# Kernel tuning notes

Measured on AMD Instinct MI355X. Metric: run time of the kernel, lower is better.

Reference implementation:

```python
import jax, jax.numpy as jnp
import numpy as np

ALPHA = 0.01  # LeakyReLU negative slope
NEG_INF = -1e12

def setup_inputs() -> dict:
    key = jax.random.key(0)
    k1, k2, k3, k4 = jax.random.split(key, 4)
    B, N, F_in, F_out = 8, 2048, 256, 128
    inp = jax.random.normal(k1, (B, N, F_in), dtype=jnp.float32)
    adj = jax.random.randint(k2, (B, N, N), 0, 2, dtype=jnp.int32)
    # xavier_uniform with gain=1.414
    limW = 1.414 * np.sqrt(6.0 / (F_in + F_out))
    W = jax.random.uniform(k3, (F_in, F_out), minval=-limW, maxval=limW, dtype=jnp.float32)
    lima = 1.414 * np.sqrt(6.0 / (2 * F_out + 1))
    a = jax.random.uniform(k4, (2 * F_out, 1), minval=-lima, maxval=lima, dtype=jnp.float32)
    return {"inp": inp, "adj": adj, "W": W, "a": a}

def reference(inp, adj, W, a):
    # h: [B, N, F_out]
    h = jnp.matmul(inp, W)
    F_out = W.shape[1]
    # Algebraic split of the attention vector: a = [a1; a2], so
    # e[b,i,j] = leakyrelu(h_i . a1 + h_j . a2)  -- avoids the O(N^2*2F) a_input.
    a1 = a[:F_out, 0]   # [F_out]
    a2 = a[F_out:, 0]   # [F_out]
    s1 = jnp.einsum('bnf,f->bn', h, a1)  # [B, N] source term
    s2 = jnp.einsum('bnf,f->bn', h, a2)  # [B, N] target term
    e = s1[:, :, None] + s2[:, None, :]  # [B, N, N]
    e = jnp.where(e > 0, e, ALPHA * e)   # leaky relu
    scores = jnp.where(adj > 0, e, NEG_INF)
    attention = jax.nn.softmax(scores, axis=2)  # [B, N, N]
    h_prime = jnp.matmul(attention, h)          # [B, N, F_out]
    return jax.nn.relu(h_prime)  # concat=True branch
```

## Files before the change

kernel.cpp:

```cpp
#include <hip/hip_runtime.h>
#include <hip/hip_bf16.h>

#define N_    2048
#define FIN   256
#define FOUT  128
#define ALPHA 0.01f

typedef short bf16x8 __attribute__((ext_vector_type(8)));
typedef float f32x4  __attribute__((ext_vector_type(4)));

static __device__ __forceinline__ unsigned short f2bf(float x) {
    __hip_bfloat16 h = __float2bfloat16(x);
    return *reinterpret_cast<unsigned short*>(&h);
}
static __device__ __forceinline__ float bf2f(unsigned short u) {
    return __uint_as_float(((unsigned)u) << 16);
}

__global__ __launch_bounds__(256) void k_wsplit(
    const float* __restrict__ W, unsigned short* __restrict__ WThi,
    unsigned short* __restrict__ WTlo)
{
    int idx = blockIdx.x * 256 + threadIdx.x;
    int k = idx >> 7, n = idx & 127;
    float w = W[k * 128 + n];
    unsigned short hi = f2bf(w);
    unsigned short lo = f2bf(w - bf2f(hi));
    WThi[n * 256 + k] = hi;
    WTlo[n * 256 + k] = lo;
}

__global__ __launch_bounds__(256) void k_pack(
    const int* __restrict__ adj, unsigned int* __restrict__ mask)
{
    __shared__ unsigned char mb[256];
    int row = blockIdx.x;
    int t = threadIdx.x;
    const int4* a4 = reinterpret_cast<const int4*>(adj + (size_t)row * N_) + 2 * t;
    int4 x = a4[0], y = a4[1];
    unsigned byte =
        (unsigned)(x.x > 0) | ((unsigned)(x.y > 0) << 1) |
        ((unsigned)(x.z > 0) << 2) | ((unsigned)(x.w > 0) << 3) |
        ((unsigned)(y.x > 0) << 4) | ((unsigned)(y.y > 0) << 5) |
        ((unsigned)(y.z > 0) << 6) | ((unsigned)(y.w > 0) << 7);
    int w = t >> 6, cig = t & 63;
    int S = cig >> 2, lg = cig & 3;
    mb[w * 64 + lg * 16 + S] = (unsigned char)byte;
    __syncthreads();
    if (t < 16)
        reinterpret_cast<uint4*>(mask)[row * 16 + t] =
            reinterpret_cast<const uint4*>(mb)[t];
}

__global__ __launch_bounds__(256) void k_lin(
    const float* __restrict__ inp,
    const unsigned short* __restrict__ WThi, const unsigned short* __restrict__ WTlo,
    const float* __restrict__ av, unsigned short* __restrict__ hT,
    float* __restrict__ s1, float* __restrict__ s2)
{
    __shared__ unsigned short Ahi[64 * 256];
    __shared__ unsigned short Alo[64 * 256];

    int g = blockIdx.x;
    int b = g & 7;
    int i0 = (g >> 3) << 6;
    int t = threadIdx.x;

    {
        int row = t >> 2;
        const float* src = inp + ((size_t)(b * N_ + i0 + row)) * FIN + (t & 3) * 64;
#pragma unroll
        for (int gseg = 0; gseg < 8; ++gseg) {
            float4 f0 = *reinterpret_cast<const float4*>(src + gseg * 8);
            float4 f1 = *reinterpret_cast<const float4*>(src + gseg * 8 + 4);
            float f[8] = {f0.x, f0.y, f0.z, f0.w, f1.x, f1.y, f1.z, f1.w};
            bf16x8 hi8, lo8;
#pragma unroll
            for (int e = 0; e < 8; ++e) {
                unsigned short h = f2bf(f[e]);
                hi8[e] = (short)h;
                lo8[e] = (short)f2bf(f[e] - bf2f(h));
            }
            int k = (t & 3) * 64 + gseg * 8;
            int off = (row * 512 + k * 2) ^ ((row & 7) << 4);
            *reinterpret_cast<bf16x8*>(reinterpret_cast<char*>(Ahi) + off) = hi8;
            *reinterpret_cast<bf16x8*>(reinterpret_cast<char*>(Alo) + off) = lo8;
        }
    }
    __syncthreads();

    int w = t >> 6, l = t & 63;
    int ln = l & 15, lg = l >> 4;
    const bf16x8* Whi8 = reinterpret_cast<const bf16x8*>(WThi);
    const bf16x8* Wlo8 = reinterpret_cast<const bf16x8*>(WTlo);

    f32x4 acc[8];
#pragma unroll
    for (int nb = 0; nb < 8; ++nb) acc[nb] = (f32x4){0.f, 0.f, 0.f, 0.f};

#pragma unroll
    for (int ks = 0; ks < 8; ++ks) {
        int arow = w * 16 + ln;
        int aoff = (arow * 512 + ks * 64 + lg * 16) ^ ((arow & 7) << 4);
        bf16x8 ahi = *reinterpret_cast<const bf16x8*>(reinterpret_cast<const char*>(Ahi) + aoff);
        bf16x8 alo = *reinterpret_cast<const bf16x8*>(reinterpret_cast<const char*>(Alo) + aoff);
#pragma unroll
        for (int nb = 0; nb < 8; ++nb) {
            int n = nb * 16 + ln;
            bf16x8 whi = Whi8[n * 32 + ks * 4 + lg];
            bf16x8 wlo = Wlo8[n * 32 + ks * 4 + lg];
            acc[nb] = __builtin_amdgcn_mfma_f32_16x16x32_bf16(ahi, whi, acc[nb], 0, 0, 0);
            acc[nb] = __builtin_amdgcn_mfma_f32_16x16x32_bf16(alo, whi, acc[nb], 0, 0, 0);
            acc[nb] = __builtin_amdgcn_mfma_f32_16x16x32_bf16(ahi, wlo, acc[nb], 0, 0, 0);
        }
    }

    float p1[4] = {0.f, 0.f, 0.f, 0.f}, p2[4] = {0.f, 0.f, 0.f, 0.f};
#pragma unroll
    for (int nb = 0; nb < 8; ++nb) {
        float a1 = av[nb * 16 + ln];
        float a2 = av[FOUT + nb * 16 + ln];
#pragma unroll
        for (int j = 0; j < 4; ++j) {
            p1[j] = fmaf(acc[nb][j], a1, p1[j]);
            p2[j] = fmaf(acc[nb][j], a2, p2[j]);
        }
    }
#pragma unroll
    for (int off = 1; off < 16; off <<= 1)
#pragma unroll
        for (int j = 0; j < 4; ++j) {
            p1[j] += __shfl_xor(p1[j], off);
            p2[j] += __shfl_xor(p2[j], off);
        }
    if (ln == 0) {
#pragma unroll
        for (int j = 0; j < 4; ++j) {
            int row = i0 + w * 16 + lg * 4 + j;
            s1[b * N_ + row] = p1[j];
            s2[b * N_ + row] = p2[j];
        }
    }

    __syncthreads();
    unsigned short* T = Ahi;
#pragma unroll
    for (int nb = 0; nb < 8; ++nb)
#pragma unroll
        for (int j = 0; j < 4; ++j)
            T[(nb * 16 + ln) * 68 + w * 16 + lg * 4 + j] = f2bf(acc[nb][j]);
    __syncthreads();
    {
        int f = t & 127, rh = t >> 7;
        unsigned short tmp[32];
#pragma unroll
        for (int c = 0; c < 32; ++c) tmp[c] = T[f * 68 + rh * 32 + c];
        int4* dst = reinterpret_cast<int4*>(&hT[((size_t)(b * FOUT + f)) * N_ + i0 + rh * 32]);
#pragma unroll
        for (int c = 0; c < 4; ++c) dst[c] = reinterpret_cast<const int4*>(tmp)[c];
    }
}

__global__ __launch_bounds__(256) void k_s2max(const float* __restrict__ s2,
                                               float* __restrict__ s2max)
{
    __shared__ float red[4];
    int b = blockIdx.x, t = threadIdx.x;
    const float4* p = reinterpret_cast<const float4*>(s2 + b * N_);
    float4 v0 = p[t], v1 = p[t + 256];
    float m = fmaxf(fmaxf(fmaxf(v0.x, v0.y), fmaxf(v0.z, v0.w)),
                    fmaxf(fmaxf(v1.x, v1.y), fmaxf(v1.z, v1.w)));
#pragma unroll
    for (int off = 1; off < 64; off <<= 1) m = fmaxf(m, __shfl_xor(m, off));
    if ((t & 63) == 0) red[t >> 6] = m;
    __syncthreads();
    if (t == 0) s2max[b] = fmaxf(fmaxf(red[0], red[1]), fmaxf(red[2], red[3]));
}

__global__ __launch_bounds__(256) void k_attn(
    const unsigned int* __restrict__ mask, const unsigned short* __restrict__ hT,
    const float* __restrict__ s1g, const float* __restrict__ s2g,
    const float* __restrict__ s2maxg, float* __restrict__ out)
{
    __shared__ float s2_lds[N_];
    __shared__ float accb[4][16][128];
    __shared__ float l_s[4][16];

    int g = blockIdx.x;
    int b = g & 7;
    int i0 = (g >> 3) << 4;
    int t = threadIdx.x;
    int w = t >> 6, l = t & 63;
    int r = l & 15, lg = l >> 4;
    int jc = w * 512;

    {
        const float4* s2g4 = reinterpret_cast<const float4*>(s2g + b * N_);
        reinterpret_cast<float4*>(s2_lds)[t] = s2g4[t];
        reinterpret_cast<float4*>(s2_lds)[t + 256] = s2g4[t + 256];
    }

    const float s1r = s1g[b * N_ + i0 + r];
    float eb = s1r + s2maxg[b];
    const float m_row = fmaxf(eb, ALPHA * eb);

    uint4 m4 = *reinterpret_cast<const uint4*>(
        reinterpret_cast<const char*>(mask) +
        ((size_t)(b * N_ + i0 + r)) * 256 + w * 64 + lg * 16);
    unsigned mw[4] = {m4.x, m4.y, m4.z, m4.w};

    const bf16x8* hvp = reinterpret_cast<const bf16x8*>(hT)
        + ((((size_t)(b * FOUT + r)) * N_ + jc + lg * 8) >> 3);

    __syncthreads();

    float l_run = 0.0f;
    f32x4 acc[8];
#pragma unroll
    for (int q = 0; q < 8; ++q) acc[q] = (f32x4){0.f, 0.f, 0.f, 0.f};

    bf16x8 h0[8], h1[8];
#pragma unroll
    for (int q = 0; q < 8; ++q) h0[q] = hvp[q * 4096];

#pragma unroll
    for (int S = 0; S < 16; ++S) {
        auto& cur = (S & 1) ? h1 : h0;
        auto& nxt = (S & 1) ? h0 : h1;
        if (S < 15) {
#pragma unroll
            for (int q = 0; q < 8; ++q) nxt[q] = hvp[q * 4096 + (S + 1) * 4];
        }
        unsigned byte = (mw[S >> 2] >> ((S & 3) * 8)) & 0xffu;
        const float* s2b = &s2_lds[jc + S * 32 + lg * 8];
        float4 ca = *reinterpret_cast<const float4*>(s2b);
        float4 cb = *reinterpret_cast<const float4*>(s2b + 4);
        float sv[8] = {ca.x, ca.y, ca.z, ca.w, cb.x, cb.y, cb.z, cb.w};

        bf16x8 af;
        float ps = 0.f;
#pragma unroll
        for (int e = 0; e < 8; ++e) {
            float v = s1r + sv[e];
            v = fmaxf(v, ALPHA * v);
            float p = (byte & (1u << e)) ? __expf(v - m_row) : 0.f;
            ps += p;
            af[e] = (short)f2bf(p);
        }
        l_run += ps;
#pragma unroll
        for (int q = 0; q < 8; ++q)
            acc[q] = __builtin_amdgcn_mfma_f32_16x16x32_bf16(af, cur[q], acc[q], 0, 0, 0);
    }

    l_run += __shfl_xor(l_run, 16);
    l_run += __shfl_xor(l_run, 32);
    if (l < 16) l_s[w][l] = l_run;

#pragma unroll
    for (int q = 0; q < 8; ++q)
#pragma unroll
        for (int rr = 0; rr < 4; ++rr)
            accb[w][lg * 4 + rr][q * 16 + r] = acc[q][rr];
    __syncthreads();

    int f = t & 127, rh = t >> 7;
#pragma unroll
    for (int rr = 0; rr < 8; ++rr) {
        int row = rh * 8 + rr;
        float L = l_s[0][row] + l_s[1][row] + l_s[2][row] + l_s[3][row];
        float v = accb[0][row][f] + accb[1][row][f] + accb[2][row][f] + accb[3][row][f];
        out[((size_t)(b * N_ + i0 + row)) * FOUT + f] = fmaxf(v / L, 0.f);
    }
}

extern "C" void kernel_launch(void* const* d_in, const int* in_sizes, int n_in,
                              void* d_out, int out_size, void* d_ws, size_t ws_size,
                              hipStream_t stream) {
    (void)in_sizes; (void)n_in; (void)out_size; (void)ws_size;
    const float* inp = (const float*)d_in[0];
    const int*   adj = (const int*)d_in[1];
    const float* W   = (const float*)d_in[2];
    const float* a   = (const float*)d_in[3];
    float* out = (float*)d_out;

    char* ws = (char*)d_ws;
    unsigned short* hT   = (unsigned short*)ws;
    unsigned int*   mask = (unsigned int*)(ws + (4u << 20));
    float* s1    = (float*)(ws + (8u << 20));
    float* s2    = s1 + 8 * N_;
    unsigned short* WThi = (unsigned short*)(s2 + 8 * N_);
    unsigned short* WTlo = WThi + FIN * FOUT;
    float* s2max = (float*)(WTlo + FIN * FOUT);

    k_wsplit<<<128, 256, 0, stream>>>(W, WThi, WTlo);
    k_pack<<<8 * N_, 256, 0, stream>>>(adj, mask);
    k_lin<<<256, 256, 0, stream>>>(inp, WThi, WTlo, a, hT, s1, s2);
    k_s2max<<<8, 256, 0, stream>>>(s2, s2max);
    k_attn<<<1024, 256, 0, stream>>>(mask, hT, s1, s2, s2max, out);
}
```

Baseline: 289.7 us.

## Tile h and W in MFMA fragment order and process 32 rows per attention block

W is pre-split into a fragment-ordered layout so each lane's bf16x8 loads are contiguous across lanes. The projection output h is written in 32-column tiles laid out to match the attention kernel's B-operand fragments, which makes those loads coalesced. The attention kernel now handles 32 query rows per block instead of 16, so each loaded h fragment feeds two MFMA chains and half as many blocks reload h. The cost is more accumulator registers, roughly double the shared memory for the reduction buffer, and fewer blocks (512) to fill the device.

```diff
diff --git a/kernel.cpp b/kernel.cpp
--- a/kernel.cpp
+++ b/kernel.cpp
@@ -18,16 +18,18 @@
 }
 
 __global__ __launch_bounds__(256) void k_wsplit(
-    const float* __restrict__ W, unsigned short* __restrict__ WThi,
-    unsigned short* __restrict__ WTlo)
+    const float* __restrict__ W, unsigned short* __restrict__ WFhi,
+    unsigned short* __restrict__ WFlo)
 {
     int idx = blockIdx.x * 256 + threadIdx.x;
     int k = idx >> 7, n = idx & 127;
     float w = W[k * 128 + n];
     unsigned short hi = f2bf(w);
     unsigned short lo = f2bf(w - bf2f(hi));
-    WThi[n * 256 + k] = hi;
-    WTlo[n * 256 + k] = lo;
+    int nb = n >> 4, ln = n & 15, ks = k >> 5, lg = (k >> 3) & 3, e = k & 7;
+    int off = (((nb * 8 + ks) * 4 + lg) * 16 + ln) * 8 + e;
+    WFhi[off] = hi;
+    WFlo[off] = lo;
 }
 
 __global__ __launch_bounds__(256) void k_pack(
@@ -54,8 +56,8 @@
 
 __global__ __launch_bounds__(256) void k_lin(
     const float* __restrict__ inp,
-    const unsigned short* __restrict__ WThi, const unsigned short* __restrict__ WTlo,
-    const float* __restrict__ av, unsigned short* __restrict__ hT,
+    const unsigned short* __restrict__ WFhi, const unsigned short* __restrict__ WFlo,
+    const float* __restrict__ av, unsigned short* __restrict__ hF,
     float* __restrict__ s1, float* __restrict__ s2)
 {
     __shared__ unsigned short Ahi[64 * 256];
@@ -91,8 +93,8 @@
 
     int w = t >> 6, l = t & 63;
     int ln = l & 15, lg = l >> 4;
-    const bf16x8* Whi8 = reinterpret_cast<const bf16x8*>(WThi);
-    const bf16x8* Wlo8 = reinterpret_cast<const bf16x8*>(WTlo);
+    const bf16x8* Wh8 = reinterpret_cast<const bf16x8*>(WFhi);
+    const bf16x8* Wl8 = reinterpret_cast<const bf16x8*>(WFlo);
 
     f32x4 acc[8];
 #pragma unroll
@@ -106,9 +108,9 @@
         bf16x8 alo = *reinterpret_cast<const bf16x8*>(reinterpret_cast<const char*>(Alo) + aoff);
 #pragma unroll
         for (int nb = 0; nb < 8; ++nb) {
-            int n = nb * 16 + ln;
-            bf16x8 whi = Whi8[n * 32 + ks * 4 + lg];
-            bf16x8 wlo = Wlo8[n * 32 + ks * 4 + lg];
+            int fi = ((nb * 8 + ks) * 4 + lg) * 16 + ln;
+            bf16x8 whi = Wh8[fi];
+            bf16x8 wlo = Wl8[fi];
             acc[nb] = __builtin_amdgcn_mfma_f32_16x16x32_bf16(ahi, whi, acc[nb], 0, 0, 0);
             acc[nb] = __builtin_amdgcn_mfma_f32_16x16x32_bf16(alo, whi, acc[nb], 0, 0, 0);
             acc[nb] = __builtin_amdgcn_mfma_f32_16x16x32_bf16(ahi, wlo, acc[nb], 0, 0, 0);
@@ -151,11 +153,12 @@
             T[(nb * 16 + ln) * 68 + w * 16 + lg * 4 + j] = f2bf(acc[nb][j]);
     __syncthreads();
     {
-        int f = t & 127, rh = t >> 7;
+        int f = t & 127, half = t >> 7;
+        int J = (i0 >> 5) + half;
         unsigned short tmp[32];
 #pragma unroll
-        for (int c = 0; c < 32; ++c) tmp[c] = T[f * 68 + rh * 32 + c];
-        int4* dst = reinterpret_cast<int4*>(&hT[((size_t)(b * FOUT + f)) * N_ + i0 + rh * 32]);
+        for (int c = 0; c < 32; ++c) tmp[c] = T[f * 68 + half * 32 + c];
+        int4* dst = reinterpret_cast<int4*>(&hF[(((size_t)(b * 64 + J)) * 128 + f) * 32]);
 #pragma unroll
         for (int c = 0; c < 4; ++c) dst[c] = reinterpret_cast<const int4*>(tmp)[c];
     }
@@ -178,17 +181,17 @@
 }
 
 __global__ __launch_bounds__(256) void k_attn(
-    const unsigned int* __restrict__ mask, const unsigned short* __restrict__ hT,
+    const unsigned int* __restrict__ mask, const unsigned short* __restrict__ hF,
     const float* __restrict__ s1g, const float* __restrict__ s2g,
     const float* __restrict__ s2maxg, float* __restrict__ out)
 {
     __shared__ float s2_lds[N_];
-    __shared__ float accb[4][16][128];
-    __shared__ float l_s[4][16];
+    __shared__ float accb[4][32][128];
+    __shared__ float l_s[4][32];
 
     int g = blockIdx.x;
     int b = g & 7;
-    int i0 = (g >> 3) << 4;
+    int i0 = (g >> 3) << 5;
     int t = threadIdx.x;
     int w = t >> 6, l = t & 63;
     int r = l & 15, lg = l >> 4;
@@ -200,74 +203,100 @@
         reinterpret_cast<float4*>(s2_lds)[t + 256] = s2g4[t + 256];
     }
 
-    const float s1r = s1g[b * N_ + i0 + r];
-    float eb = s1r + s2maxg[b];
-    const float m_row = fmaxf(eb, ALPHA * eb);
-
-    uint4 m4 = *reinterpret_cast<const uint4*>(
+    const float s2m = s2maxg[b];
+    const float s1r0 = s1g[b * N_ + i0 + r];
+    const float s1r1 = s1g[b * N_ + i0 + 16 + r];
+    float eb0 = s1r0 + s2m, eb1 = s1r1 + s2m;
+    const float m0 = fmaxf(eb0, ALPHA * eb0);
+    const float m1 = fmaxf(eb1, ALPHA * eb1);
+
+    uint4 m40 = *reinterpret_cast<const uint4*>(
         reinterpret_cast<const char*>(mask) +
         ((size_t)(b * N_ + i0 + r)) * 256 + w * 64 + lg * 16);
-    unsigned mw[4] = {m4.x, m4.y, m4.z, m4.w};
-
-    const bf16x8* hvp = reinterpret_cast<const bf16x8*>(hT)
-        + ((((size_t)(b * FOUT + r)) * N_ + jc + lg * 8) >> 3);
-
-    __syncthreads();
-
-    float l_run = 0.0f;
-    f32x4 acc[8];
-#pragma unroll
-    for (int q = 0; q < 8; ++q) acc[q] = (f32x4){0.f, 0.f, 0.f, 0.f};
-
-    bf16x8 h0[8], h1[8];
-#pragma unroll
-    for (int q = 0; q < 8; ++q) h0[q] = hvp[q * 4096];
+    uint4 m41 = *reinterpret_cast<const uint4*>(
+        reinterpret_cast<const char*>(mask) +
+        ((size_t)(b * N_ + i0 + 16 + r)) * 256 + w * 64 + lg * 16);
+    unsigned mw0[4] = {m40.x, m40.y, m40.z, m40.w};
+    unsigned mw1[4] = {m41.x, m41.y, m41.z, m41.w};
+
+    const bf16x8* hv = reinterpret_cast<const bf16x8*>(hF)
+        + (((size_t)(b * 64 + w * 16) * 128 + r) * 4 + lg);
+
+    __syncthreads();
+
+    float l0 = 0.f, l1 = 0.f;
+    f32x4 acc0[8], acc1[8];
+#pragma unroll
+    for (int q = 0; q < 8; ++q) {
+        acc0[q] = (f32x4){0.f, 0.f, 0.f, 0.f};
+        acc1[q] = (f32x4){0.f, 0.f, 0.f, 0.f};
+    }
+
+    bf16x8 hA[8], hB[8];
+#pragma unroll
+    for (int q = 0; q < 8; ++q) hA[q] = hv[q * 64];
 
 #pragma unroll
     for (int S = 0; S < 16; ++S) {
-        auto& cur = (S & 1) ? h1 : h0;
-        auto& nxt = (S & 1) ? h0 : h1;
+        auto& cur = (S & 1) ? hB : hA;
+        auto& nxt = (S & 1) ? hA : hB;
         if (S < 15) {
 #pragma unroll
-            for (int q = 0; q < 8; ++q) nxt[q] = hvp[q * 4096 + (S + 1) * 4];
-        }
-        unsigned byte = (mw[S >> 2] >> ((S & 3) * 8)) & 0xffu;
+            for (int q = 0; q < 8; ++q) nxt[q] = hv[(S + 1) * 512 + q * 64];
+        }
+        unsigned byte0 = (mw0[S >> 2] >> ((S & 3) * 8)) & 0xffu;
+        unsigned byte1 = (mw1[S >> 2] >> ((S & 3) * 8)) & 0xffu;
         const float* s2b = &s2_lds[jc + S * 32 + lg * 8];
         float4 ca = *reinterpret_cast<const float4*>(s2b);
         float4 cb = *reinterpret_cast<const float4*>(s2b + 4);
         float sv[8] = {ca.x, ca.y, ca.z, ca.w, cb.x, cb.y, cb.z, cb.w};
 
-        bf16x8 af;
-        float ps = 0.f;
+        bf16x8 af0, af1;
+        float ps0 = 0.f, ps1 = 0.f;
 #pragma unroll
         for (int e = 0; e < 8; ++e) {
-            float v = s1r + sv[e];
-            v = fmaxf(v, ALPHA * v);
-            float p = (byte & (1u << e)) ? __expf(v - m_row) : 0.f;
-            ps += p;
-            af[e] = (short)f2bf(p);
-        }
-        l_run += ps;
-#pragma unroll
-        for (int q = 0; q < 8; ++q)
-            acc[q] = __builtin_amdgcn_mfma_f32_16x16x32_bf16(af, cur[q], acc[q], 0, 0, 0);
-    }
-
-    l_run += __shfl_xor(l_run, 16);
-    l_run += __shfl_xor(l_run, 32);
-    if (l < 16) l_s[w][l] = l_run;
+            float v0 = s1r0 + sv[e];
+            v0 = fmaxf(v0, ALPHA * v0);
+            float p0 = (byte0 & (1u << e)) ? __expf(v0 - m0) : 0.f;
+            ps0 += p0;
+            af0[e] = (short)f2bf(p0);
+            float v1 = s1r1 + sv[e];
+            v1 = fmaxf(v1, ALPHA * v1);
+            float p1 = (byte1 & (1u << e)) ? __expf(v1 - m1) : 0.f;
+            ps1 += p1;
+            af1[e] = (short)f2bf(p1);
+        }
+        l0 += ps0;
+        l1 += ps1;
+#pragma unroll
+        for (int q = 0; q < 8; ++q) {
+            acc0[q] = __builtin_amdgcn_mfma_f32_16x16x32_bf16(af0, cur[q], acc0[q], 0, 0, 0);
+            acc1[q] = __builtin_amdgcn_mfma_f32_16x16x32_bf16(af1, cur[q], acc1[q], 0, 0, 0);
+        }
+    }
+
+    l0 += __shfl_xor(l0, 16);
+    l0 += __shfl_xor(l0, 32);
+    l1 += __shfl_xor(l1, 16);
+    l1 += __shfl_xor(l1, 32);
+    if (l < 16) {
+        l_s[w][l] = l0;
+        l_s[w][16 + l] = l1;
+    }
 
 #pragma unroll
     for (int q = 0; q < 8; ++q)
 #pragma unroll
-        for (int rr = 0; rr < 4; ++rr)
-            accb[w][lg * 4 + rr][q * 16 + r] = acc[q][rr];
+        for (int rr = 0; rr < 4; ++rr) {
+            accb[w][lg * 4 + rr][q * 16 + r] = acc0[q][rr];
+            accb[w][16 + lg * 4 + rr][q * 16 + r] = acc1[q][rr];
+        }
     __syncthreads();
 
     int f = t & 127, rh = t >> 7;
 #pragma unroll
-    for (int rr = 0; rr < 8; ++rr) {
-        int row = rh * 8 + rr;
+    for (int rr = 0; rr < 16; ++rr) {
+        int row = rh * 16 + rr;
         float L = l_s[0][row] + l_s[1][row] + l_s[2][row] + l_s[3][row];
         float v = accb[0][row][f] + accb[1][row][f] + accb[2][row][f] + accb[3][row][f];
         out[((size_t)(b * N_ + i0 + row)) * FOUT + f] = fmaxf(v / L, 0.f);
@@ -285,17 +314,17 @@
     float* out = (float*)d_out;
 
     char* ws = (char*)d_ws;
-    unsigned short* hT   = (unsigned short*)ws;
+    unsigned short* hF   = (unsigned short*)ws;
     unsigned int*   mask = (unsigned int*)(ws + (4u << 20));
     float* s1    = (float*)(ws + (8u << 20));
     float* s2    = s1 + 8 * N_;
-    unsigned short* WThi = (unsigned short*)(s2 + 8 * N_);
-    unsigned short* WTlo = WThi + FIN * FOUT;
-    float* s2max = (float*)(WTlo + FIN * FOUT);
-
-    k_wsplit<<<128, 256, 0, stream>>>(W, WThi, WTlo);
+    unsigned short* WFhi = (unsigned short*)(s2 + 8 * N_);
+    unsigned short* WFlo = WFhi + FIN * FOUT;
+    float* s2max = (float*)(WFlo + FIN * FOUT);
+
+    k_wsplit<<<128, 256, 0, stream>>>(W, WFhi, WFlo);
     k_pack<<<8 * N_, 256, 0, stream>>>(adj, mask);
-    k_lin<<<256, 256, 0, stream>>>(inp, WThi, WTlo, a, hT, s1, s2);
+    k_lin<<<256, 256, 0, stream>>>(inp, WFhi, WFlo, a, hF, s1, s2);
     k_s2max<<<8, 256, 0, stream>>>(s2, s2max);
-    k_attn<<<1024, 256, 0, stream>>>(mask, hT, s1, s2, s2max, out);
-}
+    k_attn<<<512, 256, 0, stream>>>(mask, hF, s1, s2, s2max, out);
+}
```

Measured after the change: 253.2 us. 1.14x faster.

## Restructure attention kernel to share h tiles across 64 rows via LDS

Applied to the files above, without the earlier changes.

The attention kernel now processes 64 rows per block, with each wave owning 16 rows over the full 2048 columns, instead of splitting columns across waves. Each block stages h chunks from global memory into double-buffered LDS, prefetching through registers, so all four waves reuse the same tile. This cuts global h traffic and removes the cross-wave LDS reduction at the end. h and W are stored in fragment-friendly layouts so loads are contiguous. The separate s2 max kernel is folded into the attention kernel. The cost is a barrier every step and fewer blocks (256).

```diff
diff --git a/kernel.cpp b/kernel.cpp
--- a/kernel.cpp
+++ b/kernel.cpp
@@ -18,16 +18,18 @@
 }
 
 __global__ __launch_bounds__(256) void k_wsplit(
-    const float* __restrict__ W, unsigned short* __restrict__ WThi,
-    unsigned short* __restrict__ WTlo)
+    const float* __restrict__ W, unsigned short* __restrict__ WFhi,
+    unsigned short* __restrict__ WFlo)
 {
     int idx = blockIdx.x * 256 + threadIdx.x;
     int k = idx >> 7, n = idx & 127;
     float w = W[k * 128 + n];
     unsigned short hi = f2bf(w);
     unsigned short lo = f2bf(w - bf2f(hi));
-    WThi[n * 256 + k] = hi;
-    WTlo[n * 256 + k] = lo;
+    int nb = n >> 4, ln = n & 15, ks = k >> 5, lg = (k >> 3) & 3, e = k & 7;
+    int off = (((nb * 8 + ks) * 4 + lg) * 16 + ln) * 8 + e;
+    WFhi[off] = hi;
+    WFlo[off] = lo;
 }
 
 __global__ __launch_bounds__(256) void k_pack(
@@ -43,9 +45,8 @@
         ((unsigned)(x.z > 0) << 2) | ((unsigned)(x.w > 0) << 3) |
         ((unsigned)(y.x > 0) << 4) | ((unsigned)(y.y > 0) << 5) |
         ((unsigned)(y.z > 0) << 6) | ((unsigned)(y.w > 0) << 7);
-    int w = t >> 6, cig = t & 63;
-    int S = cig >> 2, lg = cig & 3;
-    mb[w * 64 + lg * 16 + S] = (unsigned char)byte;
+    int S = t >> 2, lg = t & 3;
+    mb[lg * 64 + S] = (unsigned char)byte;
     __syncthreads();
     if (t < 16)
         reinterpret_cast<uint4*>(mask)[row * 16 + t] =
@@ -54,8 +55,8 @@
 
 __global__ __launch_bounds__(256) void k_lin(
     const float* __restrict__ inp,
-    const unsigned short* __restrict__ WThi, const unsigned short* __restrict__ WTlo,
-    const float* __restrict__ av, unsigned short* __restrict__ hT,
+    const unsigned short* __restrict__ WFhi, const unsigned short* __restrict__ WFlo,
+    const float* __restrict__ av, unsigned short* __restrict__ hF,
     float* __restrict__ s1, float* __restrict__ s2)
 {
     __shared__ unsigned short Ahi[64 * 256];
@@ -91,8 +92,8 @@
 
     int w = t >> 6, l = t & 63;
     int ln = l & 15, lg = l >> 4;
-    const bf16x8* Whi8 = reinterpret_cast<const bf16x8*>(WThi);
-    const bf16x8* Wlo8 = reinterpret_cast<const bf16x8*>(WTlo);
+    const bf16x8* Wh8 = reinterpret_cast<const bf16x8*>(WFhi);
+    const bf16x8* Wl8 = reinterpret_cast<const bf16x8*>(WFlo);
 
     f32x4 acc[8];
 #pragma unroll
@@ -106,9 +107,9 @@
         bf16x8 alo = *reinterpret_cast<const bf16x8*>(reinterpret_cast<const char*>(Alo) + aoff);
 #pragma unroll
         for (int nb = 0; nb < 8; ++nb) {
-            int n = nb * 16 + ln;
-            bf16x8 whi = Whi8[n * 32 + ks * 4 + lg];
-            bf16x8 wlo = Wlo8[n * 32 + ks * 4 + lg];
+            int fi = ((nb * 8 + ks) * 4 + lg) * 16 + ln;
+            bf16x8 whi = Wh8[fi];
+            bf16x8 wlo = Wl8[fi];
             acc[nb] = __builtin_amdgcn_mfma_f32_16x16x32_bf16(ahi, whi, acc[nb], 0, 0, 0);
             acc[nb] = __builtin_amdgcn_mfma_f32_16x16x32_bf16(alo, whi, acc[nb], 0, 0, 0);
             acc[nb] = __builtin_amdgcn_mfma_f32_16x16x32_bf16(ahi, wlo, acc[nb], 0, 0, 0);
@@ -151,48 +152,32 @@
             T[(nb * 16 + ln) * 68 + w * 16 + lg * 4 + j] = f2bf(acc[nb][j]);
     __syncthreads();
     {
-        int f = t & 127, rh = t >> 7;
+        int f = t & 127, half = t >> 7;
+        int J = (i0 >> 5) + half;
         unsigned short tmp[32];
 #pragma unroll
-        for (int c = 0; c < 32; ++c) tmp[c] = T[f * 68 + rh * 32 + c];
-        int4* dst = reinterpret_cast<int4*>(&hT[((size_t)(b * FOUT + f)) * N_ + i0 + rh * 32]);
+        for (int c = 0; c < 32; ++c) tmp[c] = T[f * 68 + half * 32 + c];
+        int4* dst = reinterpret_cast<int4*>(&hF[(((size_t)(b * 64 + J)) * 128 + f) * 32]);
 #pragma unroll
         for (int c = 0; c < 4; ++c) dst[c] = reinterpret_cast<const int4*>(tmp)[c];
     }
 }
 
-__global__ __launch_bounds__(256) void k_s2max(const float* __restrict__ s2,
-                                               float* __restrict__ s2max)
-{
-    __shared__ float red[4];
-    int b = blockIdx.x, t = threadIdx.x;
-    const float4* p = reinterpret_cast<const float4*>(s2 + b * N_);
-    float4 v0 = p[t], v1 = p[t + 256];
-    float m = fmaxf(fmaxf(fmaxf(v0.x, v0.y), fmaxf(v0.z, v0.w)),
-                    fmaxf(fmaxf(v1.x, v1.y), fmaxf(v1.z, v1.w)));
-#pragma unroll
-    for (int off = 1; off < 64; off <<= 1) m = fmaxf(m, __shfl_xor(m, off));
-    if ((t & 63) == 0) red[t >> 6] = m;
-    __syncthreads();
-    if (t == 0) s2max[b] = fmaxf(fmaxf(red[0], red[1]), fmaxf(red[2], red[3]));
-}
-
 __global__ __launch_bounds__(256) void k_attn(
-    const unsigned int* __restrict__ mask, const unsigned short* __restrict__ hT,
+    const unsigned int* __restrict__ mask, const unsigned short* __restrict__ hF,
     const float* __restrict__ s1g, const float* __restrict__ s2g,
-    const float* __restrict__ s2maxg, float* __restrict__ out)
+    float* __restrict__ out)
 {
     __shared__ float s2_lds[N_];
-    __shared__ float accb[4][16][128];
-    __shared__ float l_s[4][16];
+    __shared__ char  hbuf[2 * 8192];
+    __shared__ float red[4];
 
     int g = blockIdx.x;
     int b = g & 7;
-    int i0 = (g >> 3) << 4;
+    int i0 = (g >> 3) << 6;
     int t = threadIdx.x;
     int w = t >> 6, l = t & 63;
-    int r = l & 15, lg = l >> 4;
-    int jc = w * 512;
+    int ln = l & 15, lg = l >> 4;
 
     {
         const float4* s2g4 = reinterpret_cast<const float4*>(s2g + b * N_);
@@ -200,78 +185,112 @@
         reinterpret_cast<float4*>(s2_lds)[t + 256] = s2g4[t + 256];
     }
 
-    const float s1r = s1g[b * N_ + i0 + r];
-    float eb = s1r + s2maxg[b];
+    const int myrow = i0 + w * 16 + ln;
+    const float s1r = s1g[b * N_ + myrow];
+
+    const uint4* maskp4 = reinterpret_cast<const uint4*>(
+        reinterpret_cast<const char*>(mask) + ((size_t)(b * N_ + myrow)) * 256 + lg * 64);
+
+    const int toff = t * 32;
+    const int wbase = toff ^ (((((toff >> 6) ^ (toff >> 8)) & 3)) << 4);
+    const int base_r = (ln * 64 + lg * 16) ^ (((ln ^ (ln >> 2)) & 3) << 4);
+
+    const char* hF_b = reinterpret_cast<const char*>(hF) + (size_t)b * 64 * 128 * 64;
+    const char* gend = hF_b + 63 * 8192;
+
+    uint4 st[4][2];
+#pragma unroll
+    for (int k = 0; k < 4; ++k) {
+        st[k][0] = *reinterpret_cast<const uint4*>(hF_b + k * 8192 + toff);
+        st[k][1] = *reinterpret_cast<const uint4*>(hF_b + k * 8192 + toff + 16);
+    }
+    *reinterpret_cast<uint4*>(hbuf + wbase) = st[0][0];
+    *reinterpret_cast<uint4*>(hbuf + (wbase ^ 16)) = st[0][1];
+    st[0][0] = *reinterpret_cast<const uint4*>(hF_b + 4 * 8192 + toff);
+    st[0][1] = *reinterpret_cast<const uint4*>(hF_b + 4 * 8192 + toff + 16);
+    uint4 mv_cur = maskp4[0];
+
+    asm volatile("s_waitcnt lgkmcnt(0)" ::: "memory");
+    __builtin_amdgcn_s_barrier();
+
+    {
+        float4 a = *reinterpret_cast<const float4*>(&s2_lds[t * 8]);
+        float4 c = *reinterpret_cast<const float4*>(&s2_lds[t * 8 + 4]);
+        float m = fmaxf(fmaxf(fmaxf(a.x, a.y), fmaxf(a.z, a.w)),
+                        fmaxf(fmaxf(c.x, c.y), fmaxf(c.z, c.w)));
+#pragma unroll
+        for (int off = 1; off < 64; off <<= 1) m = fmaxf(m, __shfl_xor(m, off));
+        if (l == 0) red[w] = m;
+        asm volatile("s_waitcnt lgkmcnt(0)" ::: "memory");
+        __builtin_amdgcn_s_barrier();
+    }
+    const float s2m = fmaxf(fmaxf(red[0], red[1]), fmaxf(red[2], red[3]));
+    float eb = s1r + s2m;
     const float m_row = fmaxf(eb, ALPHA * eb);
 
-    uint4 m4 = *reinterpret_cast<const uint4*>(
-        reinterpret_cast<const char*>(mask) +
-        ((size_t)(b * N_ + i0 + r)) * 256 + w * 64 + lg * 16);
-    unsigned mw[4] = {m4.x, m4.y, m4.z, m4.w};
-
-    const bf16x8* hvp = reinterpret_cast<const bf16x8*>(hT)
-        + ((((size_t)(b * FOUT + r)) * N_ + jc + lg * 8) >> 3);
-
-    __syncthreads();
-
-    float l_run = 0.0f;
+    float l_run = 0.f;
     f32x4 acc[8];
 #pragma unroll
     for (int q = 0; q < 8; ++q) acc[q] = (f32x4){0.f, 0.f, 0.f, 0.f};
 
-    bf16x8 h0[8], h1[8];
-#pragma unroll
-    for (int q = 0; q < 8; ++q) h0[q] = hvp[q * 4096];
-
-#pragma unroll
-    for (int S = 0; S < 16; ++S) {
-        auto& cur = (S & 1) ? h1 : h0;
-        auto& nxt = (S & 1) ? h0 : h1;
-        if (S < 15) {
-#pragma unroll
-            for (int q = 0; q < 8; ++q) nxt[q] = hvp[q * 4096 + (S + 1) * 4];
-        }
-        unsigned byte = (mw[S >> 2] >> ((S & 3) * 8)) & 0xffu;
-        const float* s2b = &s2_lds[jc + S * 32 + lg * 8];
-        float4 ca = *reinterpret_cast<const float4*>(s2b);
-        float4 cb = *reinterpret_cast<const float4*>(s2b + 4);
-        float sv[8] = {ca.x, ca.y, ca.z, ca.w, cb.x, cb.y, cb.z, cb.w};
-
-        bf16x8 af;
-        float ps = 0.f;
-#pragma unroll
-        for (int e = 0; e < 8; ++e) {
-            float v = s1r + sv[e];
-            v = fmaxf(v, ALPHA * v);
-            float p = (byte & (1u << e)) ? __expf(v - m_row) : 0.f;
-            ps += p;
-            af[e] = (short)f2bf(p);
-        }
-        l_run += ps;
-#pragma unroll
-        for (int q = 0; q < 8; ++q)
-            acc[q] = __builtin_amdgcn_mfma_f32_16x16x32_bf16(af, cur[q], acc[q], 0, 0, 0);
+    const char* gpref = hF_b + 5 * 8192;
+
+    for (int u = 0; u < 4; ++u) {
+        uint4 mv_next = maskp4[u < 3 ? u + 1 : 3];
+        const float* s2u = &s2_lds[u * 512 + lg * 8];
+#pragma unroll
+        for (int s = 0; s < 16; ++s) {
+            const int cur = s & 1, nxt = cur ^ 1, k = (s + 1) & 3;
+            bf16x8 fr[8];
+#pragma unroll
+            for (int q = 0; q < 8; ++q)
+                fr[q] = *reinterpret_cast<const bf16x8*>(hbuf + cur * 8192 + q * 1024 + base_r);
+            *reinterpret_cast<uint4*>(hbuf + nxt * 8192 + wbase) = st[k][0];
+            *reinterpret_cast<uint4*>(hbuf + nxt * 8192 + (wbase ^ 16)) = st[k][1];
+            const char* gp = gpref > gend ? gend : gpref;
+            st[k][0] = *reinterpret_cast<const uint4*>(gp + toff);
+            st[k][1] = *reinterpret_cast<const uint4*>(gp + toff + 16);
+            gpref += 8192;
+            unsigned mm = (&mv_cur.x)[s >> 2];
+            unsigned byte = (mm >> ((s & 3) * 8)) & 0xffu;
+            float4 ca = *reinterpret_cast<const float4*>(s2u + s * 32);
+            float4 cb = *reinterpret_cast<const float4*>(s2u + s * 32 + 4);
+            float sv[8] = {ca.x, ca.y, ca.z, ca.w, cb.x, cb.y, cb.z, cb.w};
+            bf16x8 af;
+            float ps = 0.f;
+#pragma unroll
+            for (int e = 0; e < 8; ++e) {
+                float v = s1r + sv[e];
+                v = fmaxf(v, ALPHA * v);
+                float p = (byte & (1u << e)) ? __expf(v - m_row) : 0.f;
+                ps += p;
+                af[e] = (short)f2bf(p);
+            }
+            l_run += ps;
+#pragma unroll
+            for (int q = 0; q < 8; ++q)
+                acc[q] = __builtin_amdgcn_mfma_f32_16x16x32_bf16(af, fr[q], acc[q], 0, 0, 0);
+            asm volatile("s_waitcnt lgkmcnt(0)" ::: "memory");
+            __builtin_amdgcn_s_barrier();
+        }
+        mv_cur = mv_next;
     }
 
     l_run += __shfl_xor(l_run, 16);
     l_run += __shfl_xor(l_run, 32);
-    if (l < 16) l_s[w][l] = l_run;
-
+    float Lr[4];
+#pragma unroll
+    for (int rr = 0; rr < 4; ++rr)
+        Lr[rr] = __shfl(l_run, lg * 4 + rr);
+
+    float* ob = out + ((size_t)(b * N_ + i0 + w * 16)) * FOUT;
 #pragma unroll
     for (int q = 0; q < 8; ++q)
 #pragma unroll
-        for (int rr = 0; rr < 4; ++rr)
-            accb[w][lg * 4 + rr][q * 16 + r] = acc[q][rr];
-    __syncthreads();
-
-    int f = t & 127, rh = t >> 7;
-#pragma unroll
-    for (int rr = 0; rr < 8; ++rr) {
-        int row = rh * 8 + rr;
-        float L = l_s[0][row] + l_s[1][row] + l_s[2][row] + l_s[3][row];
-        float v = accb[0][row][f] + accb[1][row][f] + accb[2][row][f] + accb[3][row][f];
-        out[((size_t)(b * N_ + i0 + row)) * FOUT + f] = fmaxf(v / L, 0.f);
-    }
+        for (int rr = 0; rr < 4; ++rr) {
+            float v = acc[q][rr] / Lr[rr];
+            ob[(size_t)(lg * 4 + rr) * FOUT + q * 16 + ln] = fmaxf(v, 0.f);
+        }
 }
 
 extern "C" void kernel_launch(void* const* d_in, const int* in_sizes, int n_in,
@@ -285,17 +304,15 @@
     float* out = (float*)d_out;
 
     char* ws = (char*)d_ws;
-    unsigned short* hT   = (unsigned short*)ws;
+    unsigned short* hF   = (unsigned short*)ws;
     unsigned int*   mask = (unsigned int*)(ws + (4u << 20));
     float* s1    = (float*)(ws + (8u << 20));
     float* s2    = s1 + 8 * N_;
-    unsigned short* WThi = (unsigned short*)(s2 + 8 * N_);
-    unsigned short* WTlo = WThi + FIN * FOUT;
-    float* s2max = (float*)(WTlo + FIN * FOUT);
-
-    k_wsplit<<<128, 256, 0, stream>>>(W, WThi, WTlo);
+    unsigned short* WFhi = (unsigned short*)(s2 + 8 * N_);
+    unsigned short* WFlo = WFhi + FIN * FOUT;
+
+    k_wsplit<<<128, 256, 0, stream>>>(W, WFhi, WFlo);
     k_pack<<<8 * N_, 256, 0, stream>>>(adj, mask);
-    k_lin<<<256, 256, 0, stream>>>(inp, WThi, WTlo, a, hT, s1, s2);
-    k_s2max<<<8, 256, 0, stream>>>(s2, s2max);
-    k_attn<<<1024, 256, 0, stream>>>(mask, hT, s1, s2, s2max, out);
-}
+    k_lin<<<256, 256, 0, stream>>>(inp, WFhi, WFlo, a, hF, s1, s2);
+    k_attn<<<256, 256, 0, stream>>>(mask, hF, s1, s2, out);
+}
```

New measurement: 278.8 us. -3.8%, faster.
